# Kernel optimization log

Measured on AMD Instinct MI355X. Metric: run time of the kernel, lower is better.

Reference implementation:

```python
import jax, jax.numpy as jnp
import numpy as np
from jax.ops import segment_sum

N_NODES = 100000


def gcn_norm(edge_index, edge_weight, num_nodes):
    # Add self-loops with weight 1 (PyG gcn_norm default fill_value=1.0)
    loop = jnp.arange(num_nodes, dtype=edge_index.dtype)
    src = jnp.concatenate([edge_index[0], loop])
    dst = jnp.concatenate([edge_index[1], loop])
    w = jnp.concatenate([edge_weight, jnp.ones((num_nodes,), edge_weight.dtype)])
    deg = segment_sum(w, dst, num_segments=num_nodes)  # in-degree (col)
    dis = jnp.where(deg > 0, jax.lax.rsqrt(deg), 0.0)
    norm = dis[src] * w * dis[dst]
    return src, dst, norm


def gcn_conv(x, src, dst, norm, W, b, num_nodes):
    xw = x @ W                       # [N, out] linear first (small out dim)
    msg = xw[src] * norm[:, None]    # gather + scale, [E+N, out]
    out = segment_sum(msg, dst, num_segments=num_nodes)
    return out + b


def setup_inputs() -> dict:
    key = jax.random.key(0)
    ks = jax.random.split(key, 6)
    N, E, Cin, H, Cout = N_NODES, 3200000, 512, 16, 40
    x = jax.random.normal(ks[0], (N, Cin), dtype=jnp.float32)
    edge_index = jax.random.randint(ks[1], (2, E), 0, N, dtype=jnp.int64)
    edge_weight = jax.random.uniform(ks[2], (E,), dtype=jnp.float32)
    W1 = jax.random.normal(ks[3], (Cin, H), dtype=jnp.float32) / np.sqrt(Cin)
    b1 = jnp.zeros((H,), jnp.float32)
    W2 = jax.random.normal(ks[4], (H, Cout), dtype=jnp.float32) / np.sqrt(H)
    b2 = jnp.zeros((Cout,), jnp.float32)
    return {"x": x, "edge_index": edge_index, "edge_weight": edge_weight,
            "W1": W1, "b1": b1, "W2": W2, "b2": b2}


def reference(x, edge_index, edge_weight, W1, b1, W2, b2):
    N = x.shape[0]
    # gcn_norm computed once; GCNConv(cached=True) reuses it for both layers
    src, dst, norm = gcn_norm(edge_index, edge_weight, N)
    h = jax.nn.relu(gcn_conv(x, src, dst, norm, W1, b1, N))
    # F.dropout(training=self.training): identity in eval mode
    h = gcn_conv(h, src, dst, norm, W2, b2, N)
    return jax.nn.log_softmax(h, axis=1)
```

## Files before the change

### kernel.cpp

```cpp
#include <hip/hip_runtime.h>

#define CIN  512
#define HDIM 16
#define CODIM 40
#define BINSZ 256
#define BSHIFT 8
#define NBMAX 512
#define EB 4096
#define CAP 9216
#define CSR_CH 9
#define PADG 18

__device__ __forceinline__ void fma4(float4& a, float s, float4 b) {
  a.x = fmaf(s, b.x, a.x);
  a.y = fmaf(s, b.y, a.y);
  a.z = fmaf(s, b.z, a.z);
  a.w = fmaf(s, b.w, a.w);
}

__device__ __forceinline__ float4 red4(float4 v) {
  v.x += __shfl_xor(v.x, 1); v.y += __shfl_xor(v.y, 1);
  v.z += __shfl_xor(v.z, 1); v.w += __shfl_xor(v.w, 1);
  v.x += __shfl_xor(v.x, 2); v.y += __shfl_xor(v.y, 2);
  v.z += __shfl_xor(v.z, 2); v.w += __shfl_xor(v.w, 2);
  return v;
}

__device__ __forceinline__ float4 shx4(float4 v, int m) {
  return make_float4(__shfl_xor(v.x, m), __shfl_xor(v.y, m),
                     __shfl_xor(v.z, m), __shfl_xor(v.w, m));
}

__device__ __forceinline__ float4 bf4(ushort4 u) {
  return make_float4(__uint_as_float((unsigned)u.x << 16),
                     __uint_as_float((unsigned)u.y << 16),
                     __uint_as_float((unsigned)u.z << 16),
                     __uint_as_float((unsigned)u.w << 16));
}
__device__ __forceinline__ unsigned short f2bf(float f) {
  unsigned u = __float_as_uint(f);
  return (unsigned short)((u + 0x7FFFu + ((u >> 16) & 1u)) >> 16);
}
__device__ __forceinline__ ushort4 pk4(float4 v) {
  ushort4 r;
  r.x = f2bf(v.x); r.y = f2bf(v.y); r.z = f2bf(v.z); r.w = f2bf(v.w);
  return r;
}

__global__ void k_zero(int* __restrict__ p, int n) {
  int i = blockIdx.x * 256 + threadIdx.x;
  if (i < n) p[i] = 0;
}

__global__ __launch_bounds__(256) void k_binB(const int* __restrict__ src,
                                              const int* __restrict__ dst,
                                              const float* __restrict__ w,
                                              int* __restrict__ cursor,
                                              uint2* __restrict__ binned, int E) {
  __shared__ int hist[NBMAX];
  __shared__ int base[NBMAX];
  int t = threadIdx.x;
  for (int i = t; i < NBMAX; i += 256) hist[i] = 0;
  __syncthreads();
  int beg = blockIdx.x * EB, end = min(E, beg + EB);
  int dbuf[EB / 256];
  #pragma unroll
  for (int j = 0; j < EB / 256; ++j) {
    int e = beg + t + j * 256;
    int d = (e < end) ? dst[e] : -1;
    dbuf[j] = d;
    if (d >= 0) atomicAdd(&hist[d >> BSHIFT], 1);
  }
  __syncthreads();
  for (int i = t; i < NBMAX; i += 256) {
    int h = hist[i];
    base[i] = h ? (i * CAP + atomicAdd(&cursor[i], h)) : 0;
  }
  __syncthreads();
  #pragma unroll
  for (int j = 0; j < EB / 256; ++j) {
    int e = beg + t + j * 256;
    int d = dbuf[j];
    if (d >= 0) {
      int b = d >> BSHIFT;
      int pos = atomicAdd(&base[b], 1);
      binned[pos] = make_uint2((unsigned)src[e] | ((unsigned)(d & (BINSZ - 1)) << 17),
                               __float_as_uint(w[e]));
    }
  }
}

__global__ __launch_bounds__(256) void k_scanBins(
    const int* __restrict__ cnt, int* __restrict__ binoff,
    int* __restrict__ rowptr, int NB, int N) {
  __shared__ int ts[256];
  int t = threadIdx.x;
  int c0 = (2 * t     < NB) ? cnt[2 * t]     : 0;
  int c1 = (2 * t + 1 < NB) ? cnt[2 * t + 1] : 0;
  int s = c0 + c1;
  ts[t] = s;
  __syncthreads();
  #pragma unroll
  for (int off = 1; off < 256; off <<= 1) {
    int v = (t >= off) ? ts[t - off] : 0;
    __syncthreads();
    ts[t] += v;
    __syncthreads();
  }
  int ex = ts[t] - s;
  if (2 * t     < NB) binoff[2 * t]     = ex;
  if (2 * t + 1 < NB) binoff[2 * t + 1] = ex + c0;
  if (t == 255) { binoff[NB] = ts[255]; rowptr[N] = ts[255]; }
}

__global__ __launch_bounds__(1024) void k_csrbin(
    const int* __restrict__ binoff, const uint2* __restrict__ binned,
    int* __restrict__ rowptr, int2* __restrict__ csr,
    float* __restrict__ dis, int N) {
  __shared__ int   hist[BINSZ];
  __shared__ int   loff[BINSZ];
  __shared__ int   rank[BINSZ];
  __shared__ float dsum[BINSZ];
  int t = threadIdx.x, b = blockIdx.x;
  if (t < BINSZ) { hist[t] = 0; rank[t] = 0; dsum[t] = 1.0f; }
  __syncthreads();
  int cbeg = binoff[b], cnt = binoff[b + 1] - cbeg;
  size_t pbeg = (size_t)b * CAP;
  uint2 ebuf[CSR_CH];
  #pragma unroll
  for (int j = 0; j < CSR_CH; ++j) {
    int i = t + j * 1024;
    uint2 e = (i < cnt) ? binned[pbeg + i] : make_uint2(0u, 0u);
    ebuf[j] = e;
    if (i < cnt) {
      int dl = e.x >> 17;
      atomicAdd(&hist[dl], 1);
      atomicAdd(&dsum[dl], __uint_as_float(e.y));
    }
  }
  __syncthreads();
  if (t < BINSZ) loff[t] = hist[t];
  __syncthreads();
  #pragma unroll
  for (int off = 1; off < BINSZ; off <<= 1) {
    int v = 0;
    if (t < BINSZ && t >= off) v = loff[t - off];
    __syncthreads();
    if (t < BINSZ) loff[t] += v;
    __syncthreads();
  }
  if (t < BINSZ) {
    int ex = loff[t] - hist[t];
    int n = b * BINSZ + t;
    if (n < N) {
      rowptr[n] = cbeg + ex;
      dis[n] = rsqrtf(dsum[t]);
    }
    loff[t] = ex;
  }
  __syncthreads();
  #pragma unroll
  for (int j = 0; j < CSR_CH; ++j) {
    int i = t + j * 1024;
    if (i < cnt) {
      uint2 e = ebuf[j];
      int dl = e.x >> 17;
      int r = atomicAdd(&rank[dl], 1);
      csr[cbeg + loff[dl] + r] = make_int2((int)(e.x & 0x1FFFFu), (int)e.y);
    }
  }
}

__global__ __launch_bounds__(256) void k_gemm1(
    const float* __restrict__ x, const float* __restrict__ W1,
    const float* __restrict__ dis, unsigned short* __restrict__ y1, int N) {
  __shared__ float4 w1s[128 * PADG];
  int t = threadIdx.x;
  const float4* W14 = (const float4*)W1;
  for (int lin = t; lin < 2048; lin += 256)
    w1s[(lin >> 4) * PADG + (lin & 15)] = W14[lin];
  __syncthreads();

  int quad = t >> 2;
  int q = t & 3;
  int n0 = blockIdx.x * 128 + quad * 2;
  if (n0 >= N) return;
  bool v1 = (n0 + 1) < N;

  const float4* xA = (const float4*)x + (size_t)n0 * (CIN / 4);
  const float4* xB = xA + (CIN / 4);
  float4 z4 = make_float4(0.f, 0.f, 0.f, 0.f);
  float4 a0 = z4, a1 = z4, a2 = z4, a3 = z4;
  float4 b0 = z4, b1_ = z4, b2 = z4, b3 = z4;

  #pragma unroll 4
  for (int kk = 0; kk < 32; ++kk) {
    float4 xa = xA[kk * 4 + q];
    float4 xb = v1 ? xB[kk * 4 + q] : z4;
    const float4* wr = w1s + (kk * 4 + q) * PADG;
    float4 w0 = wr[0],  w1v = wr[1],  w2 = wr[2],  w3 = wr[3];
    fma4(a0, xa.x, w0); fma4(a1, xa.x, w1v); fma4(a2, xa.x, w2); fma4(a3, xa.x, w3);
    fma4(b0, xb.x, w0); fma4(b1_, xb.x, w1v); fma4(b2, xb.x, w2); fma4(b3, xb.x, w3);
    w0 = wr[4]; w1v = wr[5]; w2 = wr[6]; w3 = wr[7];
    fma4(a0, xa.y, w0); fma4(a1, xa.y, w1v); fma4(a2, xa.y, w2); fma4(a3, xa.y, w3);
    fma4(b0, xb.y, w0); fma4(b1_, xb.y, w1v); fma4(b2, xb.y, w2); fma4(b3, xb.y, w3);
    w0 = wr[8]; w1v = wr[9]; w2 = wr[10]; w3 = wr[11];
    fma4(a0, xa.z, w0); fma4(a1, xa.z, w1v); fma4(a2, xa.z, w2); fma4(a3, xa.z, w3);
    fma4(b0, xb.z, w0); fma4(b1_, xb.z, w1v); fma4(b2, xb.z, w2); fma4(b3, xb.z, w3);
    w0 = wr[12]; w1v = wr[13]; w2 = wr[14]; w3 = wr[15];
    fma4(a0, xa.w, w0); fma4(a1, xa.w, w1v); fma4(a2, xa.w, w2); fma4(a3, xa.w, w3);
    fma4(b0, xb.w, w0); fma4(b1_, xb.w, w1v); fma4(b2, xb.w, w2); fma4(b3, xb.w, w3);
  }
  a0 = red4(a0); a1 = red4(a1); a2 = red4(a2); a3 = red4(a3);
  b0 = red4(b0); b1_ = red4(b1_); b2 = red4(b2); b3 = red4(b3);

  float dA = dis[n0];
  float4 sA = (q == 0) ? a0 : (q == 1) ? a1 : (q == 2) ? a2 : a3;
  sA.x *= dA; sA.y *= dA; sA.z *= dA; sA.w *= dA;
  ((ushort4*)y1)[(size_t)n0 * 4 + q] = pk4(sA);
  if (v1) {
    float dB = dis[n0 + 1];
    float4 sB = (q == 0) ? b0 : (q == 1) ? b1_ : (q == 2) ? b2 : b3;
    sB.x *= dB; sB.y *= dB; sB.z *= dB; sB.w *= dB;
    ((ushort4*)y1)[(size_t)(n0 + 1) * 4 + q] = pk4(sB);
  }
}

__device__ __forceinline__ float4 rowAccB(const int2* __restrict__ csr,
                                          const ushort4* __restrict__ v4,
                                          float4 s0, int beg, int end, int q) {
  float4 s1 = make_float4(0.f, 0.f, 0.f, 0.f), s2 = s1, s3 = s1;
  int i = beg;
  for (; i + 3 < end; i += 4) {
    int2 e0 = csr[i], e1 = csr[i + 1], e2 = csr[i + 2], e3 = csr[i + 3];
    ushort4 u0 = v4[(size_t)e0.x * 4 + q];
    ushort4 u1 = v4[(size_t)e1.x * 4 + q];
    ushort4 u2 = v4[(size_t)e2.x * 4 + q];
    ushort4 u3 = v4[(size_t)e3.x * 4 + q];
    fma4(s0, __int_as_float(e0.y), bf4(u0));
    fma4(s1, __int_as_float(e1.y), bf4(u1));
    fma4(s2, __int_as_float(e2.y), bf4(u2));
    fma4(s3, __int_as_float(e3.y), bf4(u3));
  }
  for (; i < end; ++i) {
    int2 e = csr[i];
    fma4(s0, __int_as_float(e.y), bf4(v4[(size_t)e.x * 4 + q]));
  }
  s0.x += s1.x + s2.x + s3.x;
  s0.y += s1.y + s2.y + s3.y;
  s0.z += s1.z + s2.z + s3.z;
  s0.w += s1.w + s2.w + s3.w;
  return s0;
}

__global__ __launch_bounds__(256) void k_aggZ(
    const int* __restrict__ rowptr, const int2* __restrict__ csr,
    const unsigned short* __restrict__ vals, unsigned short* __restrict__ zb,
    const float* __restrict__ dis, const float* __restrict__ b1, int N) {
  int t = threadIdx.x;
  int node = blockIdx.x * 64 + (t >> 2);
  int q = t & 3;
  if (node >= N) return;
  const ushort4* v4 = (const ushort4*)vals;
  float4 a = rowAccB(csr, v4, bf4(v4[(size_t)node * 4 + q]),
                     rowptr[node], rowptr[node + 1], q);
  float d = dis[node];
  float4 bb = ((const float4*)b1)[q];
  float4 z;
  z.x = d * fmaxf(fmaf(d, a.x, bb.x), 0.f);
  z.y = d * fmaxf(fmaf(d, a.y, bb.y), 0.f);
  z.z = d * fmaxf(fmaf(d, a.z, bb.z), 0.f);
  z.w = d * fmaxf(fmaf(d, a.w, bb.w), 0.f);
  ((ushort4*)zb)[(size_t)node * 4 + q] = pk4(z);
}

__global__ __launch_bounds__(256) void k_aggF(
    const int* __restrict__ rowptr, const int2* __restrict__ csr,
    const unsigned short* __restrict__ vals, float* __restrict__ out,
    const float* __restrict__ dis, const float* __restrict__ W2,
    const float* __restrict__ b2, int N) {
  __shared__ float w2s[HDIM * CODIM + CODIM];
  int t = threadIdx.x;
  for (int i = t; i < HDIM * CODIM; i += 256) w2s[i] = W2[i];
  if (t < CODIM) w2s[HDIM * CODIM + t] = b2[t];
  __syncthreads();

  int node = blockIdx.x * 64 + (t >> 2);
  int q = t & 3;
  if (node >= N) return;
  const ushort4* v4 = (const ushort4*)vals;
  float4 a = rowAccB(csr, v4, bf4(v4[(size_t)node * 4 + q]),
                     rowptr[node], rowptr[node + 1], q);
  float d = dis[node];
  a.x *= d; a.y *= d; a.z *= d; a.w *= d;

  float4 f1 = shx4(a, 1), f2 = shx4(a, 2), f3 = shx4(a, 3);

  int col0 = q * 10;
  float v[10];
  #pragma unroll
  for (int jj = 0; jj < 10; ++jj) v[jj] = w2s[HDIM * CODIM + col0 + jj];

  {
    const float* wr;
    wr = w2s + ((q ^ 0) * 4 + 0) * CODIM + col0;
    #pragma unroll
    for (int jj = 0; jj < 10; ++jj) v[jj] = fmaf(a.x, wr[jj], v[jj]);
    wr = w2s + ((q ^ 0) * 4 + 1) * CODIM + col0;
    #pragma unroll
    for (int jj = 0; jj < 10; ++jj) v[jj] = fmaf(a.y, wr[jj], v[jj]);
    wr = w2s + ((q ^ 0) * 4 + 2) * CODIM + col0;
    #pragma unroll
    for (int jj = 0; jj < 10; ++jj) v[jj] = fmaf(a.z, wr[jj], v[jj]);
    wr = w2s + ((q ^ 0) * 4 + 3) * CODIM + col0;
    #pragma unroll
    for (int jj = 0; jj < 10; ++jj) v[jj] = fmaf(a.w, wr[jj], v[jj]);

    wr = w2s + ((q ^ 1) * 4 + 0) * CODIM + col0;
    #pragma unroll
    for (int jj = 0; jj < 10; ++jj) v[jj] = fmaf(f1.x, wr[jj], v[jj]);
    wr = w2s + ((q ^ 1) * 4 + 1) * CODIM + col0;
    #pragma unroll
    for (int jj = 0; jj < 10; ++jj) v[jj] = fmaf(f1.y, wr[jj], v[jj]);
    wr = w2s + ((q ^ 1) * 4 + 2) * CODIM + col0;
    #pragma unroll
    for (int jj = 0; jj < 10; ++jj) v[jj] = fmaf(f1.z, wr[jj], v[jj]);
    wr = w2s + ((q ^ 1) * 4 + 3) * CODIM + col0;
    #pragma unroll
    for (int jj = 0; jj < 10; ++jj) v[jj] = fmaf(f1.w, wr[jj], v[jj]);

    wr = w2s + ((q ^ 2) * 4 + 0) * CODIM + col0;
    #pragma unroll
    for (int jj = 0; jj < 10; ++jj) v[jj] = fmaf(f2.x, wr[jj], v[jj]);
    wr = w2s + ((q ^ 2) * 4 + 1) * CODIM + col0;
    #pragma unroll
    for (int jj = 0; jj < 10; ++jj) v[jj] = fmaf(f2.y, wr[jj], v[jj]);
    wr = w2s + ((q ^ 2) * 4 + 2) * CODIM + col0;
    #pragma unroll
    for (int jj = 0; jj < 10; ++jj) v[jj] = fmaf(f2.z, wr[jj], v[jj]);
    wr = w2s + ((q ^ 2) * 4 + 3) * CODIM + col0;
    #pragma unroll
    for (int jj = 0; jj < 10; ++jj) v[jj] = fmaf(f2.w, wr[jj], v[jj]);

    wr = w2s + ((q ^ 3) * 4 + 0) * CODIM + col0;
    #pragma unroll
    for (int jj = 0; jj < 10; ++jj) v[jj] = fmaf(f3.x, wr[jj], v[jj]);
    wr = w2s + ((q ^ 3) * 4 + 1) * CODIM + col0;
    #pragma unroll
    for (int jj = 0; jj < 10; ++jj) v[jj] = fmaf(f3.y, wr[jj], v[jj]);
    wr = w2s + ((q ^ 3) * 4 + 2) * CODIM + col0;
    #pragma unroll
    for (int jj = 0; jj < 10; ++jj) v[jj] = fmaf(f3.z, wr[jj], v[jj]);
    wr = w2s + ((q ^ 3) * 4 + 3) * CODIM + col0;
    #pragma unroll
    for (int jj = 0; jj < 10; ++jj) v[jj] = fmaf(f3.w, wr[jj], v[jj]);
  }

  float m = v[0];
  #pragma unroll
  for (int jj = 1; jj < 10; ++jj) m = fmaxf(m, v[jj]);
  m = fmaxf(m, __shfl_xor(m, 1));
  m = fmaxf(m, __shfl_xor(m, 2));
  float sum = 0.f;
  #pragma unroll
  for (int jj = 0; jj < 10; ++jj) sum += __expf(v[jj] - m);
  sum += __shfl_xor(sum, 1);
  sum += __shfl_xor(sum, 2);
  float lse = __logf(sum) + m;
  float* o = out + (size_t)node * CODIM + col0;
  #pragma unroll
  for (int jj = 0; jj < 10; ++jj) o[jj] = v[jj] - lse;
}

extern "C" void kernel_launch(void* const* d_in, const int* in_sizes, int n_in,
                              void* d_out, int out_size, void* d_ws, size_t ws_size,
                              hipStream_t stream) {
  const float* x  = (const float*)d_in[0];
  const int*   ei = (const int*)d_in[1];
  const float* ew = (const float*)d_in[2];
  const float* W1 = (const float*)d_in[3];
  const float* b1 = (const float*)d_in[4];
  const float* W2 = (const float*)d_in[5];
  const float* b2 = (const float*)d_in[6];
  float* out = (float*)d_out;

  int N = in_sizes[0] / CIN;
  int E = in_sizes[2];
  const int* src = ei;
  const int* dst = ei + E;
  int NB = (N + BINSZ - 1) >> BSHIFT;

  size_t NA = ((size_t)N + 255) & ~(size_t)255;
  size_t NP = ((size_t)N + 2) & ~(size_t)1;
  int*   cursor = (int*)d_ws;
  int*   binoff = cursor + NBMAX;
  int*   rowptr = binoff + NBMAX + 4;
  int2*  csr    = (int2*)(rowptr + NP);
  float* dis    = (float*)(csr + E);
  unsigned short* zb = (unsigned short*)(dis + NA);
  uint2* binned = (uint2*)(zb + NA * 16);
  unsigned short* y1 = (unsigned short*)binned;

  int gG   = (N + 63) / 64;
  int gG2  = (N + 127) / 128;
  int gEB  = (E + EB - 1) / EB;

  k_zero    <<<(NB + 255) / 256, 256, 0, stream>>>(cursor, NB);
  k_binB    <<<gEB, 256, 0, stream>>>(src, dst, ew, cursor, binned, E);
  k_scanBins<<<1, 256, 0, stream>>>(cursor, binoff, rowptr, NB, N);
  k_csrbin  <<<NB, 1024, 0, stream>>>(binoff, binned, rowptr, csr, dis, N);

  k_gemm1   <<<gG2, 256, 0, stream>>>(x, W1, dis, y1, N);
  k_aggZ    <<<gG, 256, 0, stream>>>(rowptr, csr, y1, zb, dis, b1, N);
  k_aggF    <<<gG, 256, 0, stream>>>(rowptr, csr, zb, out, dis, W2, b2, N);
}
```

Before: 299.7 us.

## Compute layer-1 GEMM with one node per thread and global W1 reads

Rewrites the x·W1 kernel so each thread computes all 16 outputs for one node. The LDS staging of W1 and the cross-lane shuffle reduction are gone, and W1 is read directly from global memory with uniform addresses. Outputs are packed to bf16 and written as two 16-byte stores. This removes shuffles and the LDS/sync work, but each thread now streams its own 2 KB row, so loads are strided across the wavefront and less coalesced, and fewer blocks are launched.

```diff
diff --git a/kernel.cpp b/kernel.cpp
--- a/kernel.cpp
+++ b/kernel.cpp
@@ -9,7 +9,6 @@
 #define EB 4096
 #define CAP 9216
 #define CSR_CH 9
-#define PADG 18
 
 __device__ __forceinline__ void fma4(float4& a, float s, float4 b) {
   a.x = fmaf(s, b.x, a.x);
@@ -18,14 +17,6 @@
   a.w = fmaf(s, b.w, a.w);
 }
 
-__device__ __forceinline__ float4 red4(float4 v) {
-  v.x += __shfl_xor(v.x, 1); v.y += __shfl_xor(v.y, 1);
-  v.z += __shfl_xor(v.z, 1); v.w += __shfl_xor(v.w, 1);
-  v.x += __shfl_xor(v.x, 2); v.y += __shfl_xor(v.y, 2);
-  v.z += __shfl_xor(v.z, 2); v.w += __shfl_xor(v.w, 2);
-  return v;
-}
-
 __device__ __forceinline__ float4 shx4(float4 v, int m) {
   return make_float4(__shfl_xor(v.x, m), __shfl_xor(v.y, m),
                      __shfl_xor(v.z, m), __shfl_xor(v.w, m));
@@ -45,6 +36,9 @@
   ushort4 r;
   r.x = f2bf(v.x); r.y = f2bf(v.y); r.z = f2bf(v.z); r.w = f2bf(v.w);
   return r;
+}
+__device__ __forceinline__ unsigned pk2(float lo, float hi) {
+  return (unsigned)f2bf(lo) | ((unsigned)f2bf(hi) << 16);
 }
 
 __global__ void k_zero(int* __restrict__ p, int n) {
@@ -174,56 +168,44 @@
 __global__ __launch_bounds__(256) void k_gemm1(
     const float* __restrict__ x, const float* __restrict__ W1,
     const float* __restrict__ dis, unsigned short* __restrict__ y1, int N) {
-  __shared__ float4 w1s[128 * PADG];
-  int t = threadIdx.x;
-  const float4* W14 = (const float4*)W1;
-  for (int lin = t; lin < 2048; lin += 256)
-    w1s[(lin >> 4) * PADG + (lin & 15)] = W14[lin];
-  __syncthreads();
-
-  int quad = t >> 2;
-  int q = t & 3;
-  int n0 = blockIdx.x * 128 + quad * 2;
-  if (n0 >= N) return;
-  bool v1 = (n0 + 1) < N;
-
-  const float4* xA = (const float4*)x + (size_t)n0 * (CIN / 4);
-  const float4* xB = xA + (CIN / 4);
-  float4 z4 = make_float4(0.f, 0.f, 0.f, 0.f);
-  float4 a0 = z4, a1 = z4, a2 = z4, a3 = z4;
-  float4 b0 = z4, b1_ = z4, b2 = z4, b3 = z4;
-
-  #pragma unroll 4
-  for (int kk = 0; kk < 32; ++kk) {
-    float4 xa = xA[kk * 4 + q];
-    float4 xb = v1 ? xB[kk * 4 + q] : z4;
-    const float4* wr = w1s + (kk * 4 + q) * PADG;
-    float4 w0 = wr[0],  w1v = wr[1],  w2 = wr[2],  w3 = wr[3];
-    fma4(a0, xa.x, w0); fma4(a1, xa.x, w1v); fma4(a2, xa.x, w2); fma4(a3, xa.x, w3);
-    fma4(b0, xb.x, w0); fma4(b1_, xb.x, w1v); fma4(b2, xb.x, w2); fma4(b3, xb.x, w3);
-    w0 = wr[4]; w1v = wr[5]; w2 = wr[6]; w3 = wr[7];
-    fma4(a0, xa.y, w0); fma4(a1, xa.y, w1v); fma4(a2, xa.y, w2); fma4(a3, xa.y, w3);
-    fma4(b0, xb.y, w0); fma4(b1_, xb.y, w1v); fma4(b2, xb.y, w2); fma4(b3, xb.y, w3);
-    w0 = wr[8]; w1v = wr[9]; w2 = wr[10]; w3 = wr[11];
-    fma4(a0, xa.z, w0); fma4(a1, xa.z, w1v); fma4(a2, xa.z, w2); fma4(a3, xa.z, w3);
-    fma4(b0, xb.z, w0); fma4(b1_, xb.z, w1v); fma4(b2, xb.z, w2); fma4(b3, xb.z, w3);
-    w0 = wr[12]; w1v = wr[13]; w2 = wr[14]; w3 = wr[15];
-    fma4(a0, xa.w, w0); fma4(a1, xa.w, w1v); fma4(a2, xa.w, w2); fma4(a3, xa.w, w3);
-    fma4(b0, xb.w, w0); fma4(b1_, xb.w, w1v); fma4(b2, xb.w, w2); fma4(b3, xb.w, w3);
-  }
-  a0 = red4(a0); a1 = red4(a1); a2 = red4(a2); a3 = red4(a3);
-  b0 = red4(b0); b1_ = red4(b1_); b2 = red4(b2); b3 = red4(b3);
-
-  float dA = dis[n0];
-  float4 sA = (q == 0) ? a0 : (q == 1) ? a1 : (q == 2) ? a2 : a3;
-  sA.x *= dA; sA.y *= dA; sA.z *= dA; sA.w *= dA;
-  ((ushort4*)y1)[(size_t)n0 * 4 + q] = pk4(sA);
-  if (v1) {
-    float dB = dis[n0 + 1];
-    float4 sB = (q == 0) ? b0 : (q == 1) ? b1_ : (q == 2) ? b2 : b3;
-    sB.x *= dB; sB.y *= dB; sB.z *= dB; sB.w *= dB;
-    ((ushort4*)y1)[(size_t)(n0 + 1) * 4 + q] = pk4(sB);
-  }
+  int n = blockIdx.x * 256 + threadIdx.x;
+  if (n >= N) return;
+  const float4* xr = (const float4*)x + (size_t)n * (CIN / 4);
+  const float4* W4 = (const float4*)W1;
+  float4 a0 = make_float4(0.f, 0.f, 0.f, 0.f), a1 = a0, a2 = a0, a3 = a0;
+
+  for (int kb = 0; kb < 128; kb += 8) {
+    float4 xv[8];
+    #pragma unroll
+    for (int j = 0; j < 8; ++j) xv[j] = xr[kb + j];
+    #pragma unroll
+    for (int j = 0; j < 8; ++j) {
+      int k0 = (kb + j) * 4;
+      const float4* wr = W4 + (size_t)k0 * 4;
+      fma4(a0, xv[j].x, wr[0]);  fma4(a1, xv[j].x, wr[1]);
+      fma4(a2, xv[j].x, wr[2]);  fma4(a3, xv[j].x, wr[3]);
+      fma4(a0, xv[j].y, wr[4]);  fma4(a1, xv[j].y, wr[5]);
+      fma4(a2, xv[j].y, wr[6]);  fma4(a3, xv[j].y, wr[7]);
+      fma4(a0, xv[j].z, wr[8]);  fma4(a1, xv[j].z, wr[9]);
+      fma4(a2, xv[j].z, wr[10]); fma4(a3, xv[j].z, wr[11]);
+      fma4(a0, xv[j].w, wr[12]); fma4(a1, xv[j].w, wr[13]);
+      fma4(a2, xv[j].w, wr[14]); fma4(a3, xv[j].w, wr[15]);
+    }
+  }
+
+  float d = dis[n];
+  a0.x *= d; a0.y *= d; a0.z *= d; a0.w *= d;
+  a1.x *= d; a1.y *= d; a1.z *= d; a1.w *= d;
+  a2.x *= d; a2.y *= d; a2.z *= d; a2.w *= d;
+  a3.x *= d; a3.y *= d; a3.z *= d; a3.w *= d;
+
+  uint4 P0, P1;
+  P0.x = pk2(a0.x, a0.y); P0.y = pk2(a0.z, a0.w);
+  P0.z = pk2(a1.x, a1.y); P0.w = pk2(a1.z, a1.w);
+  P1.x = pk2(a2.x, a2.y); P1.y = pk2(a2.z, a2.w);
+  P1.z = pk2(a3.x, a3.y); P1.w = pk2(a3.z, a3.w);
+  ((uint4*)y1)[(size_t)n * 2 + 0] = P0;
+  ((uint4*)y1)[(size_t)n * 2 + 1] = P1;
 }
 
 __device__ __forceinline__ float4 rowAccB(const int2* __restrict__ csr,
@@ -402,7 +384,7 @@
   unsigned short* y1 = (unsigned short*)binned;
 
   int gG   = (N + 63) / 64;
-  int gG2  = (N + 127) / 128;
+  int gN   = (N + 255) / 256;
   int gEB  = (E + EB - 1) / EB;
 
   k_zero    <<<(NB + 255) / 256, 256, 0, stream>>>(cursor, NB);
@@ -410,7 +392,7 @@
   k_scanBins<<<1, 256, 0, stream>>>(cursor, binoff, rowptr, NB, N);
   k_csrbin  <<<NB, 1024, 0, stream>>>(binoff, binned, rowptr, csr, dis, N);
 
-  k_gemm1   <<<gG2, 256, 0, stream>>>(x, W1, dis, y1, N);
+  k_gemm1   <<<gN, 256, 0, stream>>>(x, W1, dis, y1, N);
   k_aggZ    <<<gG, 256, 0, stream>>>(rowptr, csr, y1, zb, dis, b1, N);
   k_aggF    <<<gG, 256, 0, stream>>>(rowptr, csr, zb, out, dis, W2, b2, N);
 }
```

Result: faster. 293.0 us (-2.2%).
